# Performance work log

Hardware: AMD Instinct MI355X
Metric: run time of the kernel (lower is better)

## Reference

```python
import jax, jax.numpy as jnp
import numpy as np

B, S, D = 8, 2048, 1024


def setup_inputs() -> dict:
    key = jax.random.key(0)
    ks = jax.random.split(key, 9)
    s = 1.0 / np.sqrt(D)
    return {
        "x": jax.random.normal(ks[0], (B, S, D), dtype=jnp.float32),
        "Wq": jax.random.normal(ks[1], (D, D), dtype=jnp.float32) * s,
        "bq": jnp.zeros((D,), dtype=jnp.float32),
        "Wk": jax.random.normal(ks[2], (D, D), dtype=jnp.float32) * s,
        "bk": jnp.zeros((D,), dtype=jnp.float32),
        "Wv": jax.random.normal(ks[3], (D, D), dtype=jnp.float32) * s,
        "bv": jnp.zeros((D,), dtype=jnp.float32),
        "Wo": jax.random.normal(ks[4], (D, D), dtype=jnp.float32) * s,
        "bo": jnp.zeros((D,), dtype=jnp.float32),
    }


def reference(x, Wq, bq, Wk, bk, Wv, bv, Wo, bo):
    # Single-head self-attention with full NxN scores (as in the torch module).
    q = jnp.einsum("bsd,de->bse", x, Wq) + bq
    k = jnp.einsum("bsd,de->bse", x, Wk) + bk
    v = jnp.einsum("bsd,de->bse", x, Wv) + bv
    scores = jnp.einsum("bqd,bkd->bqk", q, k) / jnp.sqrt(jnp.float32(D))
    attn = jax.nn.softmax(scores, axis=-1)
    y = jnp.einsum("bqk,bkd->bqd", attn, v)
    return jnp.einsum("bsd,de->bse", y, Wo) + bo
```

## Files before the change

kernel.cpp:

```cpp
#include <hip/hip_runtime.h>
#include <stdint.h>


using u16 = unsigned short;
using u32 = unsigned int;
using short8  = __attribute__((ext_vector_type(8))) short;
using floatx4 = __attribute__((ext_vector_type(4))) float;

#define GPTR(p) ((__attribute__((address_space(1))) u32*)(p))
#define LPTR(p) ((__attribute__((address_space(3))) u32*)(p))
#define MFMA16 __builtin_amdgcn_mfma_f32_16x16x32_bf16

__device__ __forceinline__ void async_cp16(const void* g, void* l) {
  __builtin_amdgcn_global_load_lds(GPTR(g), LPTR(l), 16, 0, 0);
}

__device__ __forceinline__ u16 f2bf(float f) {
  u32 u = __builtin_bit_cast(u32, f);
  u = (u + 0x7fffu + ((u >> 16) & 1u)) >> 16;
  return (u16)u;
}
__device__ __forceinline__ float bf2f(u16 h) {
  u32 u = ((u32)h) << 16;
  return __builtin_bit_cast(float, u);
}

__device__ __forceinline__ void swz(int gx, int gy, int& bx, int& by) {
  int s = blockIdx.x + gx * blockIdx.y;
  int q = s >> 3;
  by = (s & 7) * (gy >> 3) + q / gx;
  bx = q % gx;
}

__device__ __forceinline__ void gemm_core(
    const u16* __restrict__ A, const u16* __restrict__ B,
    int lda, int ldb, int K, u16* lA, u16* lB, floatx4 acc[4][4])
{
  const int tid  = threadIdx.x;
  const int lane = tid & 63;
  const int w    = tid >> 6;
  const int r8   = lane >> 3;
  const int cg   = (lane & 7) ^ r8;
  const int frow = lane & 15;
  const int fq   = lane >> 4;
  const int wrow = (w >> 1) * 64;
  const int wcol = (w & 1) * 64;

  const u16* gaL = A + (size_t)(w * 32 + r8) * lda + cg * 8;
  const u16* gbL = B + (size_t)(w * 32 + r8) * ldb + cg * 8;
  u16* lAw = lA + (w * 32) * 64;
  u16* lBw = lB + (w * 32) * 64;
  const int x0 = ((0 + fq) ^ (frow & 7)) * 8;
  const int x1 = ((4 + fq) ^ (frow & 7)) * 8;

  for (int k0 = 0; k0 < K; k0 += 64) {
    const u16* ga = gaL + k0;
    const u16* gb = gbL + k0;
#pragma unroll
    for (int t = 0; t < 4; ++t) {
      async_cp16(ga + (size_t)(t * 8) * lda, lAw + t * 8 * 64);
      async_cp16(gb + (size_t)(t * 8) * ldb, lBw + t * 8 * 64);
    }
    __syncthreads();

#pragma unroll
    for (int sub = 0; sub < 2; ++sub) {
      const int xs = sub ? x1 : x0;
      short8 af[4], bfr[4];
#pragma unroll
      for (int i = 0; i < 4; ++i)
        af[i] = *(const short8*)(lA + (wrow + i * 16 + frow) * 64 + xs);
#pragma unroll
      for (int j = 0; j < 4; ++j)
        bfr[j] = *(const short8*)(lB + (wcol + j * 16 + frow) * 64 + xs);
#pragma unroll
      for (int i = 0; i < 4; ++i)
#pragma unroll
        for (int j = 0; j < 4; ++j)
          acc[i][j] = MFMA16(af[i], bfr[j], acc[i][j], 0, 0, 0);
    }
    __syncthreads();
  }
}

__device__ __forceinline__ void gemm256(
    const u16* __restrict__ A, const u16* __restrict__ B,
    int lda, int ldb, int K, u16* smem, floatx4 acc[8][4])
{
  const int tid  = threadIdx.x;
  const int lane = tid & 63;
  const int w    = tid >> 6;
  const int frow = lane & 15;
  const int fq   = lane >> 4;
  const int wrow = (w >> 2) * 128;
  const int wcol = (w & 3) * 64;
  const int x0 = ((0 + fq) ^ (frow & 7)) * 8;
  const int x1 = ((4 + fq) ^ (frow & 7)) * 8;
  const int sr = tid >> 3, sl = tid & 7;
  const size_t aoff = (size_t)sr * lda + ((sl ^ (sr & 7)) << 3);
  const size_t boff = (size_t)sr * ldb + ((sl ^ (sr & 7)) << 3);
  const int nt = K >> 6;

  auto stage = [&](int t, int bsel) {
    const u16* ga = A + t * 64 + aoff;
    const u16* gb = B + t * 64 + boff;
    u16* la = smem + bsel * 16384 + tid * 8;
    u16* lb = smem + 32768 + bsel * 16384 + tid * 8;
#pragma unroll
    for (int q = 0; q < 4; ++q)
      async_cp16(ga + (size_t)(q * 64) * lda, la + q * 4096);
#pragma unroll
    for (int q = 0; q < 4; ++q)
      async_cp16(gb + (size_t)(q * 64) * ldb, lb + q * 4096);
  };

  stage(0, 0);
  if (nt > 1) stage(1, 1);

  for (int t = 0; t < nt; ++t) {
    const u16* la = smem + (t & 1) * 16384;
    const u16* lb = smem + 32768 + (t & 1) * 16384;
    if (t + 1 < nt) { asm volatile("s_waitcnt vmcnt(8)" ::: "memory"); }
    else            { asm volatile("s_waitcnt vmcnt(0)" ::: "memory"); }
    __builtin_amdgcn_s_barrier();

    short8 af[4][2], b0[2][2], b1[2][2];
#pragma unroll
    for (int i = 0; i < 4; ++i) {
      af[i][0] = *(const short8*)(la + (wrow + i * 16 + frow) * 64 + x0);
      af[i][1] = *(const short8*)(la + (wrow + i * 16 + frow) * 64 + x1);
    }
#pragma unroll
    for (int j = 0; j < 2; ++j) {
      b0[j][0] = *(const short8*)(lb + (wcol + j * 16 + frow) * 64 + x0);
      b0[j][1] = *(const short8*)(lb + (wcol + j * 16 + frow) * 64 + x1);
    }
    __builtin_amdgcn_s_setprio(1);
#pragma unroll
    for (int i = 0; i < 4; ++i)
#pragma unroll
      for (int j = 0; j < 2; ++j) {
        acc[i][j] = MFMA16(af[i][0], b0[j][0], acc[i][j], 0, 0, 0);
        acc[i][j] = MFMA16(af[i][1], b0[j][1], acc[i][j], 0, 0, 0);
      }
    __builtin_amdgcn_s_setprio(0);
#pragma unroll
    for (int j = 0; j < 2; ++j) {
      b1[j][0] = *(const short8*)(lb + (wcol + (2 + j) * 16 + frow) * 64 + x0);
      b1[j][1] = *(const short8*)(lb + (wcol + (2 + j) * 16 + frow) * 64 + x1);
    }
    __builtin_amdgcn_s_setprio(1);
#pragma unroll
    for (int i = 0; i < 4; ++i)
#pragma unroll
      for (int j = 0; j < 2; ++j) {
        acc[i][2 + j] = MFMA16(af[i][0], b1[j][0], acc[i][2 + j], 0, 0, 0);
        acc[i][2 + j] = MFMA16(af[i][1], b1[j][1], acc[i][2 + j], 0, 0, 0);
      }
    __builtin_amdgcn_s_setprio(0);
#pragma unroll
    for (int i = 0; i < 4; ++i) {
      af[i][0] = *(const short8*)(la + (wrow + (4 + i) * 16 + frow) * 64 + x0);
      af[i][1] = *(const short8*)(la + (wrow + (4 + i) * 16 + frow) * 64 + x1);
    }
    __builtin_amdgcn_s_setprio(1);
#pragma unroll
    for (int i = 0; i < 4; ++i)
#pragma unroll
      for (int j = 0; j < 2; ++j) {
        acc[4 + i][2 + j] = MFMA16(af[i][0], b1[j][0], acc[4 + i][2 + j], 0, 0, 0);
        acc[4 + i][2 + j] = MFMA16(af[i][1], b1[j][1], acc[4 + i][2 + j], 0, 0, 0);
      }
    __builtin_amdgcn_s_setprio(0);
    __builtin_amdgcn_s_setprio(1);
#pragma unroll
    for (int i = 0; i < 4; ++i)
#pragma unroll
      for (int j = 0; j < 2; ++j) {
        acc[4 + i][j] = MFMA16(af[i][0], b0[j][0], acc[4 + i][j], 0, 0, 0);
        acc[4 + i][j] = MFMA16(af[i][1], b0[j][1], acc[4 + i][j], 0, 0, 0);
      }
    __builtin_amdgcn_s_setprio(0);

    __builtin_amdgcn_s_barrier();
    if (t + 2 < nt) stage(t + 2, t & 1);
  }
}

__global__ __launch_bounds__(256) void k_cast_x(const float* __restrict__ x, u16* __restrict__ xb) {
  size_t i = ((size_t)blockIdx.x * 256 + threadIdx.x) * 8;
  float4 a = *(const float4*)(x + i);
  float4 b = *(const float4*)(x + i + 4);
  u16 o[8] __attribute__((aligned(16)));
  o[0] = f2bf(a.x); o[1] = f2bf(a.y); o[2] = f2bf(a.z); o[3] = f2bf(a.w);
  o[4] = f2bf(b.x); o[5] = f2bf(b.y); o[6] = f2bf(b.z); o[7] = f2bf(b.w);
  *(uint4*)(xb + i) = *(const uint4*)o;
}

__global__ __launch_bounds__(256) void k_cast_wt(
    const float* __restrict__ Wq, const float* __restrict__ Wk,
    const float* __restrict__ Wo, const float* __restrict__ Wv,
    u16* __restrict__ WT, u16* __restrict__ Wvb)
{
  __shared__ float t[32][33];
  const int z = blockIdx.z;
  const int c = threadIdx.x & 31, r = threadIdx.x >> 5;
  if (z == 3) {
#pragma unroll
    for (int p = 0; p < 4; ++p) {
      const size_t idx = (size_t)(blockIdx.y * 32 + r + 8 * p) * 1024 + blockIdx.x * 32 + c;
      Wvb[idx] = f2bf(Wv[idx]);
    }
    return;
  }
  const float* W = (z == 0) ? Wq : (z == 1) ? Wk : Wo;
  u16* out = WT + (size_t)z * 1024 * 1024;
#pragma unroll
  for (int p = 0; p < 4; ++p)
    t[r + 8 * p][c] = W[(size_t)(blockIdx.y * 32 + r + 8 * p) * 1024 + blockIdx.x * 32 + c];
  __syncthreads();
#pragma unroll
  for (int p = 0; p < 4; ++p)
    out[(size_t)(blockIdx.x * 32 + r + 8 * p) * 1024 + blockIdx.y * 32 + c] = f2bf(t[c][r + 8 * p]);
}

__global__ __launch_bounds__(256) void k_bvo(
    const float* __restrict__ bv, const float* __restrict__ Wo, float* __restrict__ bvo)
{
  const int nb = blockIdx.x & 3, jc = blockIdx.x >> 2;
  const int n = nb * 256 + threadIdx.x;
  float s = 0.f;
#pragma unroll 4
  for (int j = jc * 64; j < jc * 64 + 64; ++j) s += bv[j] * Wo[(size_t)j * 1024 + n];
  atomicAdd(&bvo[n], s);
}

__global__ __launch_bounds__(256, 4) void k_wvo_part(
    const u16* __restrict__ WoT, const u16* __restrict__ Wvb, float* __restrict__ Pf)
{
  __shared__ u16 lA[8192], lB[8192];
  const int bx = blockIdx.x, by = blockIdx.y, z = blockIdx.z;
  const u16* Am = WoT + (size_t)by * 128 * 1024 + z * 256;
  const u16* Bm = Wvb + (size_t)bx * 128 * 1024 + z * 256;
  floatx4 acc[4][4] = {};
  gemm_core(Am, Bm, 1024, 1024, 256, lA, lB, acc);

  float* out = Pf + (size_t)z * 1024 * 1024;
  const int lane = threadIdx.x & 63, w = threadIdx.x >> 6;
  const int wrow = (w >> 1) * 64, wcol = (w & 1) * 64;
#pragma unroll
  for (int j = 0; j < 4; ++j) {
    const int c = bx * 128 + wcol + j * 16 + (lane & 15);
#pragma unroll
    for (int i = 0; i < 4; ++i) {
      const int m0 = by * 128 + wrow + i * 16 + (lane >> 4) * 4;
#pragma unroll
      for (int r = 0; r < 4; ++r)
        out[(size_t)(m0 + r) * 1024 + c] = acc[i][j][r];
    }
  }
}

__global__ __launch_bounds__(256) void k_wvo_red(
    const float* __restrict__ Pf, u16* __restrict__ WvoT)
{
  const size_t e = ((size_t)blockIdx.x * 256 + threadIdx.x) * 8;
  u16 o[8] __attribute__((aligned(16)));
#pragma unroll
  for (int h = 0; h < 2; ++h) {
    float4 s = *(const float4*)(Pf + e + h * 4);
#pragma unroll
    for (int z = 1; z < 4; ++z) {
      float4 p = *(const float4*)(Pf + (size_t)z * 1024 * 1024 + e + h * 4);
      s.x += p.x; s.y += p.y; s.z += p.z; s.w += p.w;
    }
    o[h * 4 + 0] = f2bf(s.x); o[h * 4 + 1] = f2bf(s.y);
    o[h * 4 + 2] = f2bf(s.z); o[h * 4 + 3] = f2bf(s.w);
  }
  *(uint4*)(WvoT + e) = *(const uint4*)o;
}

__global__ __launch_bounds__(512, 2) void k_qkv2(
    const u16* __restrict__ XB, const u16* __restrict__ WT,
    const float* __restrict__ bq, const float* __restrict__ bk, const float* __restrict__ bvo,
    u16* __restrict__ Q, u16* __restrict__ Kb, u16* __restrict__ Vt)
{
  extern __shared__ __align__(16) u16 smem[];
  int bx, by; swz(4, 64, bx, by);
  const int mode = blockIdx.z;
  const u16* Am = XB + (size_t)by * 256 * 1024;
  const int ws_idx = (mode == 2) ? 3 : mode;
  const u16* Bm = WT + (size_t)ws_idx * 1024 * 1024 + (size_t)bx * 256 * 1024;
  const float* bias = (mode == 0) ? bq : (mode == 1) ? bk : bvo;
  floatx4 acc[8][4] = {};
  gemm256(Am, Bm, 1024, 1024, 1024, smem, acc);

  const int tid = threadIdx.x, lane = tid & 63, w = tid >> 6;
  const int frow = lane & 15, fq = lane >> 4;
  const int wrow = (w >> 2) * 128, wcol = (w & 3) * 64;

  if (mode == 2) {
    u16* scr = smem + w * 8192;
#pragma unroll
    for (int j = 0; j < 4; ++j) {
      const int dl = j * 16 + frow;
      const float bb = bias[bx * 256 + wcol + dl];
#pragma unroll
      for (int i = 0; i < 8; ++i) {
        const int sl_ = i * 16 + fq * 4;
        const u32 lo = (u32)f2bf(acc[i][j][0]  + bb) | ((u32)f2bf(acc[i][j][1] + bb) << 16);
        const u32 hi = (u32)f2bf(acc[i][j][2]  + bb) | ((u32)f2bf(acc[i][j][3] + bb) << 16);
        u32* p = (u32*)(scr + dl * 128 + (((sl_ >> 3) ^ (dl & 15)) << 3) + (sl_ & 7));
        p[0] = lo; p[1] = hi;
      }
    }
    const int b = by >> 3, s0 = (by & 7) * 256;
    const int dq = lane >> 4, cc = lane & 15;
#pragma unroll
    for (int it = 0; it < 16; ++it) {
      const int dl = it * 4 + dq;
      uint4 v = *(const uint4*)(scr + dl * 128 + ((cc ^ (dl & 15)) << 3));
      *(uint4*)(Vt + ((size_t)(b * 1024 + bx * 256 + wcol + dl)) * 2048 + s0 + wrow + cc * 8) = v;
    }
    return;
  }

#pragma unroll
  for (int j = 0; j < 4; ++j) {
    const int c = bx * 256 + wcol + j * 16 + frow;
    const float bb = bias[c];
#pragma unroll
    for (int i = 0; i < 8; ++i) {
      const int m0 = by * 256 + wrow + i * 16 + fq * 4;
#pragma unroll
      for (int r = 0; r < 4; ++r) {
        const float v = acc[i][j][r] + bb;
        if (mode == 0) Q[(size_t)(m0 + r) * 1024 + c] = f2bf(v * 0.03125f);
        else           Kb[(size_t)(m0 + r) * 1024 + c] = f2bf(v);
      }
    }
  }
}

__global__ __launch_bounds__(512, 2) void k_scores2(
    const u16* __restrict__ Q, const u16* __restrict__ Kb, u16* __restrict__ P,
    float* __restrict__ rowsum)
{
  extern __shared__ __align__(16) u16 smem[];
  const int id = blockIdx.x;
  const int b = id & 7, rest = id >> 3;
  const int bx = rest & 7, by = rest >> 3;
  const u16* Am = Q  + (size_t)b * 2048 * 1024 + (size_t)by * 256 * 1024;
  const u16* Bm = Kb + (size_t)b * 2048 * 1024 + (size_t)bx * 256 * 1024;
  floatx4 acc[8][4] = {};
  gemm256(Am, Bm, 1024, 1024, 1024, smem, acc);

  u16* Pb = P + (size_t)b * 2048 * 2048;
  const int lane = threadIdx.x & 63, w = threadIdx.x >> 6;
  const int frow = lane & 15, fq = lane >> 4;
  const int wrow = (w >> 2) * 128, wcol = (w & 3) * 64;
#pragma unroll
  for (int i = 0; i < 8; ++i) {
#pragma unroll
    for (int r = 0; r < 4; ++r) {
      const int m = by * 256 + wrow + i * 16 + fq * 4 + r;
      float part = 0.f;
#pragma unroll
      for (int j = 0; j < 4; ++j) {
        const int c = bx * 256 + wcol + j * 16 + frow;
        const float e = __expf(acc[i][j][r]);
        const u16 h = f2bf(e);
        Pb[(size_t)m * 2048 + c] = h;
        part += bf2f(h);
      }
      part += __shfl_xor(part, 1, 64);
      part += __shfl_xor(part, 2, 64);
      part += __shfl_xor(part, 4, 64);
      part += __shfl_xor(part, 8, 64);
      if (frow == 0) atomicAdd(&rowsum[b * 2048 + m], part);
    }
  }
}

__global__ __launch_bounds__(512, 2) void k_pv2(
    const u16* __restrict__ P, const u16* __restrict__ Vt,
    const float* __restrict__ bo, const float* __restrict__ rowsum,
    float* __restrict__ out)
{
  extern __shared__ __align__(16) u16 smem[];
  const int id = blockIdx.x;
  const int b = id & 7, rest = id >> 3;
  const int bx = rest & 3, by = rest >> 2;
  const u16* Am = P  + (size_t)b * 2048 * 2048 + (size_t)by * 256 * 2048;
  const u16* Bm = Vt + (size_t)b * 1024 * 2048 + (size_t)bx * 256 * 2048;
  floatx4 acc[8][4] = {};
  gemm256(Am, Bm, 2048, 2048, 2048, smem, acc);

  float* outb = out + (size_t)b * 2048 * 1024;
  const int lane = threadIdx.x & 63, w = threadIdx.x >> 6;
  const int frow = lane & 15, fq = lane >> 4;
  const int wrow = (w >> 2) * 128, wcol = (w & 3) * 64;
  float bb[4];
#pragma unroll
  for (int j = 0; j < 4; ++j) bb[j] = bo[bx * 256 + wcol + j * 16 + frow];
#pragma unroll
  for (int i = 0; i < 8; ++i) {
#pragma unroll
    for (int r = 0; r < 4; ++r) {
      const int m = by * 256 + wrow + i * 16 + fq * 4 + r;
      const float inv = 1.0f / rowsum[b * 2048 + m];
#pragma unroll
      for (int j = 0; j < 4; ++j) {
        const int c = bx * 256 + wcol + j * 16 + frow;
        outb[(size_t)m * 1024 + c] = acc[i][j][r] * inv + bb[j];
      }
    }
  }
}

extern "C" void kernel_launch(void* const* d_in, const int* in_sizes, int n_in,
                              void* d_out, int out_size, void* d_ws, size_t ws_size,
                              hipStream_t stream) {
  const float* x  = (const float*)d_in[0];
  const float* Wq = (const float*)d_in[1];
  const float* bq = (const float*)d_in[2];
  const float* Wk = (const float*)d_in[3];
  const float* bk = (const float*)d_in[4];
  const float* Wv = (const float*)d_in[5];
  const float* bv = (const float*)d_in[6];
  const float* Wo = (const float*)d_in[7];
  const float* bo = (const float*)d_in[8];
  float* out = (float*)d_out;

  char* ws = (char*)d_ws;
  u16* XB  = (u16*)(ws + 0);
  u16* WT  = (u16*)(ws + 33554432);
  u16* Q   = (u16*)(ws + 41943040);
  u16* Kb  = (u16*)(ws + 75497472);
  u16* Vt  = (u16*)(ws + 109051904);
  u16* P   = (u16*)(ws + 142606336);
  u16* Wvb = Kb;
  float* bvo    = (float*)P;
  float* WvoPf  = (float*)(ws + 142606336 + 4194304);
  float* rowsum = (float*)XB;

  if (ws_size < 209715200) return;

  static int attr_set = 0;
  if (!attr_set) {
    hipFuncSetAttribute(reinterpret_cast<const void*>(k_qkv2),
                        hipFuncAttributeMaxDynamicSharedMemorySize, 131072);
    hipFuncSetAttribute(reinterpret_cast<const void*>(k_scores2),
                        hipFuncAttributeMaxDynamicSharedMemorySize, 131072);
    hipFuncSetAttribute(reinterpret_cast<const void*>(k_pv2),
                        hipFuncAttributeMaxDynamicSharedMemorySize, 131072);
    attr_set = 1;
  }

  k_cast_wt  <<<dim3(32, 32, 4), 256, 0, stream>>>(Wq, Wk, Wo, Wv, WT, Wvb);
  k_cast_x   <<<8192, 256, 0, stream>>>(x, XB);
  hipMemsetAsync(bvo, 0, 1024 * sizeof(float), stream);
  k_bvo      <<<64, 256, 0, stream>>>(bv, Wo, bvo);
  k_wvo_part <<<dim3(8, 8, 4), 256, 0, stream>>>(WT + (size_t)2 * 1024 * 1024, Wvb, WvoPf);
  k_wvo_red  <<<512, 256, 0, stream>>>(WvoPf, WT + (size_t)3 * 1024 * 1024);
  k_qkv2     <<<dim3(4, 64, 3), 512, 131072, stream>>>(XB, WT, bq, bk, bvo, Q, Kb, Vt);
  hipMemsetAsync(rowsum, 0, 16384 * sizeof(float), stream);
  k_scores2  <<<512, 512, 131072, stream>>>(Q, Kb, P, rowsum);
  k_pv2      <<<256, 512, 131072, stream>>>(P, Vt, bo, rowsum, out);
}
```

Before: 427.8 us.

## Interleave half-tile async loads with MFMA phases in gemm256 pipeline

```diff
diff --git a/kernel.cpp b/kernel.cpp
--- a/kernel.cpp
+++ b/kernel.cpp
@@ -92,98 +92,124 @@
   const int w    = tid >> 6;
   const int frow = lane & 15;
   const int fq   = lane >> 4;
-  const int wrow = (w >> 2) * 128;
-  const int wcol = (w & 3) * 64;
+  const int ha   = w >> 2;
+  const int hb   = (w & 3) >> 1;
+  const int brow = (w & 1) * 64;
   const int x0 = ((0 + fq) ^ (frow & 7)) * 8;
   const int x1 = ((4 + fq) ^ (frow & 7)) * 8;
   const int sr = tid >> 3, sl = tid & 7;
-  const size_t aoff = (size_t)sr * lda + ((sl ^ (sr & 7)) << 3);
-  const size_t boff = (size_t)sr * ldb + ((sl ^ (sr & 7)) << 3);
+  const int csw = (sl ^ (sr & 7)) << 3;
   const int nt = K >> 6;
 
-  auto stage = [&](int t, int bsel) {
-    const u16* ga = A + t * 64 + aoff;
-    const u16* gb = B + t * 64 + boff;
-    u16* la = smem + bsel * 16384 + tid * 8;
-    u16* lb = smem + 32768 + bsel * 16384 + tid * 8;
-#pragma unroll
-    for (int q = 0; q < 4; ++q)
-      async_cp16(ga + (size_t)(q * 64) * lda, la + q * 4096);
-#pragma unroll
-    for (int q = 0; q < 4; ++q)
-      async_cp16(gb + (size_t)(q * 64) * ldb, lb + q * 4096);
+  auto stgA = [&](int t, int h, int s) {
+    const u16* g = A + (size_t)(h * 128 + sr) * lda + t * 64 + csw;
+    u16* l = smem + s * 16384 + h * 8192 + tid * 8;
+    async_cp16(g, l);
+    async_cp16(g + (size_t)64 * lda, l + 4096);
   };
-
-  stage(0, 0);
-  if (nt > 1) stage(1, 1);
-
+  auto stgB = [&](int t, int h, int s) {
+    const u16* g = B + (size_t)(h * 128 + sr) * ldb + t * 64 + csw;
+    u16* l = smem + 32768 + s * 16384 + h * 8192 + tid * 8;
+    async_cp16(g, l);
+    async_cp16(g + (size_t)64 * ldb, l + 4096);
+  };
+
+  stgA(0, 0, 0); stgA(0, 1, 0); stgB(0, 0, 0); stgB(0, 1, 0);
+  if (nt > 1) {
+    stgB(1, 0, 1); stgA(1, 0, 1);
+    asm volatile("s_waitcnt vmcnt(4)" ::: "memory");
+  } else {
+    asm volatile("s_waitcnt vmcnt(0)" ::: "memory");
+  }
+  __builtin_amdgcn_s_barrier();
+
+#pragma unroll 2
   for (int t = 0; t < nt; ++t) {
-    const u16* la = smem + (t & 1) * 16384;
-    const u16* lb = smem + 32768 + (t & 1) * 16384;
-    if (t + 1 < nt) { asm volatile("s_waitcnt vmcnt(8)" ::: "memory"); }
-    else            { asm volatile("s_waitcnt vmcnt(0)" ::: "memory"); }
-    __builtin_amdgcn_s_barrier();
-
+    const int cur = t & 1, oth = cur ^ 1;
+    const u16* lA = smem + cur * 16384 + ha * 8192;
+    const u16* lB = smem + 32768 + cur * 16384 + hb * 8192;
     short8 af[4][2], b0[2][2], b1[2][2];
+
 #pragma unroll
     for (int i = 0; i < 4; ++i) {
-      af[i][0] = *(const short8*)(la + (wrow + i * 16 + frow) * 64 + x0);
-      af[i][1] = *(const short8*)(la + (wrow + i * 16 + frow) * 64 + x1);
+      af[i][0] = *(const short8*)(lA + (i * 16 + frow) * 64 + x0);
+      af[i][1] = *(const short8*)(lA + (i * 16 + frow) * 64 + x1);
     }
 #pragma unroll
     for (int j = 0; j < 2; ++j) {
-      b0[j][0] = *(const short8*)(lb + (wcol + j * 16 + frow) * 64 + x0);
-      b0[j][1] = *(const short8*)(lb + (wcol + j * 16 + frow) * 64 + x1);
-    }
+      b0[j][0] = *(const short8*)(lB + (brow + j * 16 + frow) * 64 + x0);
+      b0[j][1] = *(const short8*)(lB + (brow + j * 16 + frow) * 64 + x1);
+    }
+    if (t + 1 < nt) stgA(t + 1, 1, oth);
+    asm volatile("s_waitcnt lgkmcnt(8)" ::: "memory");
+    __builtin_amdgcn_s_barrier();
+    asm volatile("s_waitcnt lgkmcnt(0)" ::: "memory");
     __builtin_amdgcn_s_setprio(1);
 #pragma unroll
-    for (int i = 0; i < 4; ++i)
-#pragma unroll
-      for (int j = 0; j < 2; ++j) {
-        acc[i][j] = MFMA16(af[i][0], b0[j][0], acc[i][j], 0, 0, 0);
-        acc[i][j] = MFMA16(af[i][1], b0[j][1], acc[i][j], 0, 0, 0);
-      }
+    for (int kk = 0; kk < 2; ++kk)
+#pragma unroll
+      for (int i = 0; i < 4; ++i)
+#pragma unroll
+        for (int j = 0; j < 2; ++j)
+          acc[i][j] = MFMA16(af[i][kk], b0[j][kk], acc[i][j], 0, 0, 0);
     __builtin_amdgcn_s_setprio(0);
+    __builtin_amdgcn_s_barrier();
+
 #pragma unroll
     for (int j = 0; j < 2; ++j) {
-      b1[j][0] = *(const short8*)(lb + (wcol + (2 + j) * 16 + frow) * 64 + x0);
-      b1[j][1] = *(const short8*)(lb + (wcol + (2 + j) * 16 + frow) * 64 + x1);
-    }
+      b1[j][0] = *(const short8*)(lB + (brow + 32 + j * 16 + frow) * 64 + x0);
+      b1[j][1] = *(const short8*)(lB + (brow + 32 + j * 16 + frow) * 64 + x1);
+    }
+    if (t + 1 < nt) stgB(t + 1, 1, oth);
+    __builtin_amdgcn_s_barrier();
+    asm volatile("s_waitcnt lgkmcnt(0)" ::: "memory");
     __builtin_amdgcn_s_setprio(1);
 #pragma unroll
-    for (int i = 0; i < 4; ++i)
-#pragma unroll
-      for (int j = 0; j < 2; ++j) {
-        acc[i][2 + j] = MFMA16(af[i][0], b1[j][0], acc[i][2 + j], 0, 0, 0);
-        acc[i][2 + j] = MFMA16(af[i][1], b1[j][1], acc[i][2 + j], 0, 0, 0);
-      }
+    for (int kk = 0; kk < 2; ++kk)
+#pragma unroll
+      for (int i = 0; i < 4; ++i)
+#pragma unroll
+        for (int j = 0; j < 2; ++j)
+          acc[i][2 + j] = MFMA16(af[i][kk], b1[j][kk], acc[i][2 + j], 0, 0, 0);
     __builtin_amdgcn_s_setprio(0);
+    __builtin_amdgcn_s_barrier();
+
 #pragma unroll
     for (int i = 0; i < 4; ++i) {
-      af[i][0] = *(const short8*)(la + (wrow + (4 + i) * 16 + frow) * 64 + x0);
-      af[i][1] = *(const short8*)(la + (wrow + (4 + i) * 16 + frow) * 64 + x1);
-    }
+      af[i][0] = *(const short8*)(lA + (64 + i * 16 + frow) * 64 + x0);
+      af[i][1] = *(const short8*)(lA + (64 + i * 16 + frow) * 64 + x1);
+    }
+    if (t + 2 < nt) stgB(t + 2, 0, cur);
+    __builtin_amdgcn_s_barrier();
+    asm volatile("s_waitcnt lgkmcnt(0)" ::: "memory");
     __builtin_amdgcn_s_setprio(1);
 #pragma unroll
-    for (int i = 0; i < 4; ++i)
-#pragma unroll
-      for (int j = 0; j < 2; ++j) {
-        acc[4 + i][2 + j] = MFMA16(af[i][0], b1[j][0], acc[4 + i][2 + j], 0, 0, 0);
-        acc[4 + i][2 + j] = MFMA16(af[i][1], b1[j][1], acc[4 + i][2 + j], 0, 0, 0);
-      }
+    for (int kk = 0; kk < 2; ++kk)
+#pragma unroll
+      for (int i = 0; i < 4; ++i)
+#pragma unroll
+        for (int j = 0; j < 2; ++j)
+          acc[4 + i][2 + j] = MFMA16(af[i][kk], b1[j][kk], acc[4 + i][2 + j], 0, 0, 0);
     __builtin_amdgcn_s_setprio(0);
+    __builtin_amdgcn_s_barrier();
+
+    if (t + 2 < nt) {
+      stgA(t + 2, 0, cur);
+      asm volatile("s_waitcnt vmcnt(4)" ::: "memory");
+    } else if (t + 1 < nt) {
+      asm volatile("s_waitcnt vmcnt(0)" ::: "memory");
+    }
+    __builtin_amdgcn_s_barrier();
     __builtin_amdgcn_s_setprio(1);
 #pragma unroll
-    for (int i = 0; i < 4; ++i)
-#pragma unroll
-      for (int j = 0; j < 2; ++j) {
-        acc[4 + i][j] = MFMA16(af[i][0], b0[j][0], acc[4 + i][j], 0, 0, 0);
-        acc[4 + i][j] = MFMA16(af[i][1], b0[j][1], acc[4 + i][j], 0, 0, 0);
-      }
+    for (int kk = 0; kk < 2; ++kk)
+#pragma unroll
+      for (int i = 0; i < 4; ++i)
+#pragma unroll
+        for (int j = 0; j < 2; ++j)
+          acc[4 + i][j] = MFMA16(af[i][kk], b0[j][kk], acc[4 + i][j], 0, 0, 0);
     __builtin_amdgcn_s_setprio(0);
-
-    __builtin_amdgcn_s_barrier();
-    if (t + 2 < nt) stage(t + 2, t & 1);
+    __builtin_amdgcn_s_barrier();
   }
 }
 
@@ -325,18 +351,20 @@
     return;
   }
 
-#pragma unroll
-  for (int j = 0; j < 4; ++j) {
-    const int c = bx * 256 + wcol + j * 16 + frow;
-    const float bb = bias[c];
-#pragma unroll
-    for (int i = 0; i < 8; ++i) {
-      const int m0 = by * 256 + wrow + i * 16 + fq * 4;
-#pragma unroll
-      for (int r = 0; r < 4; ++r) {
-        const float v = acc[i][j][r] + bb;
-        if (mode == 0) Q[(size_t)(m0 + r) * 1024 + c] = f2bf(v * 0.03125f);
-        else           Kb[(size_t)(m0 + r) * 1024 + c] = f2bf(v);
+  float bb4[4];
+#pragma unroll
+  for (int j = 0; j < 4; ++j) bb4[j] = bias[bx * 256 + wcol + j * 16 + frow];
+#pragma unroll
+  for (int i = 0; i < 8; ++i) {
+#pragma unroll
+    for (int r = 0; r < 4; ++r) {
+      const size_t m = (size_t)(by * 256 + wrow + i * 16 + fq * 4 + r);
+#pragma unroll
+      for (int j = 0; j < 4; ++j) {
+        const int c = bx * 256 + wcol + j * 16 + frow;
+        const float v = acc[i][j][r] + bb4[j];
+        if (mode == 0) Q[m * 1024 + c] = f2bf(v * 0.03125f);
+        else           Kb[m * 1024 + c] = f2bf(v);
       }
     }
   }
```

After: 402.3 us. 6.0% less time.
